# Performance work log

Measured on AMD Instinct MI355X. Metric: run time of the kernel, lower is better.

Reference implementation:

```python
import jax, jax.numpy as jnp
import numpy as np

ALPHA = 100.0
EPS = 1e-12  # matches torch F.normalize eps


def l2norm(v, axis):
    n = jnp.linalg.norm(v, axis=axis, keepdims=True)
    return v / jnp.maximum(n, EPS)


def setup_inputs() -> dict:
    key = jax.random.key(0)
    k1, k2 = jax.random.split(key)
    x = jax.random.normal(k1, (32, 512, 32, 32), dtype=jnp.float32)
    vocabs = jax.random.uniform(k2, (64, 512), dtype=jnp.float32)  # torch.rand init
    return {"x": x, "vocabs": vocabs}


def reference(x, vocabs):
    # x: [N, C, H, W]; vocabs: [K, C]
    N, C, H, W = x.shape
    K = vocabs.shape[0]
    x = l2norm(x, axis=1)                       # normalize descriptors over C
    xf = x.reshape(N, C, H * W)                 # [N, C, P]

    # 1x1 conv with weight = 2*alpha*vocabs, bias = -alpha*||vocabs||
    w = 2.0 * ALPHA * vocabs                    # [K, C]
    b = -ALPHA * jnp.linalg.norm(vocabs, axis=1)  # [K]
    logits = jnp.einsum('ncp,kc->nkp', xf, w) + b[None, :, None]
    a = jax.nn.softmax(logits, axis=1)          # soft assignment over K

    # Distributive rewrite of sum_p a[n,k,p]*(x[n,c,p] - vocabs[k,c])
    vlad = jnp.einsum('nkp,ncp->nkc', a, xf) - a.sum(-1)[:, :, None] * vocabs[None]
    vlad = l2norm(vlad, axis=2)                 # intra-normalization
    vlad = vlad.reshape(N, K * C)
    return l2norm(vlad, axis=1)
```

## Files before the change

kernel.cpp:

```cpp
#include <hip/hip_runtime.h>
#include <math.h>
#include <stdint.h>

#define ALPHA 100.0f
#define EPSN 1e-12f

typedef __attribute__((ext_vector_type(8))) short bf16x8;
typedef __attribute__((ext_vector_type(16))) float f32x16;
typedef __attribute__((ext_vector_type(4))) unsigned int u32x4;

static __device__ __forceinline__ uint32_t f2bf(float f) {
    uint32_t u = __builtin_bit_cast(uint32_t, f);
    return (u + 0x7FFFu + ((u >> 16) & 1u)) >> 16;
}
static __device__ __forceinline__ float bfhi(uint32_t u) {
    return __builtin_bit_cast(float, u & 0xFFFF0000u);
}
static __device__ __forceinline__ float bflo(uint32_t u) {
    return __builtin_bit_cast(float, u << 16);
}
static __device__ __forceinline__ uint32_t stage1(float f) {
    uint32_t hi = f2bf(f);
    uint32_t lo = f2bf(f - __builtin_bit_cast(float, hi << 16));
    return (hi << 16) | lo;
}
static __device__ __forceinline__ uint32_t packbf(float a, float b) {
    return f2bf(a) | (f2bf(b) << 16);
}
static __device__ __forceinline__ void lds_barrier() {
    asm volatile("s_waitcnt lgkmcnt(0)\n\ts_barrier" ::: "memory");
}

__global__ __launch_bounds__(64) void prep_kernel(const float* __restrict__ v,
                                                  unsigned short* __restrict__ vh,
                                                  unsigned short* __restrict__ vl,
                                                  float* __restrict__ bias,
                                                  float* __restrict__ az) {
    int k = blockIdx.x, lane = threadIdx.x;
    az[k * 64 + lane] = 0.f;
    const float* row = v + k * 512;
    float ssq = 0.f;
#pragma unroll
    for (int i = 0; i < 8; ++i) {
        int c = lane + 64 * i;
        float f = row[c];
        ssq = fmaf(f, f, ssq);
        uint32_t hi = f2bf(f);
        uint32_t lo = f2bf(f - __builtin_bit_cast(float, hi << 16));
        vh[k * 512 + c] = (unsigned short)hi;
        vl[k * 512 + c] = (unsigned short)lo;
    }
#pragma unroll
    for (int off = 32; off > 0; off >>= 1) ssq += __shfl_xor(ssq, off, 64);
    if (lane == 0) bias[k] = -ALPHA * sqrtf(ssq);
}

static __device__ __forceinline__ void a_load(float4& pxa, float4& pxb,
                                              u32x4& pvh, u32x4& pvl,
                                              const float* xg,
                                              const unsigned short* vhg,
                                              const unsigned short* vlg,
                                              int c0, int xr, int xq) {
    pxa = *(const float4*)(xg + (size_t)(c0 + xr) * 1024 + xq);
    pxb = *(const float4*)(xg + (size_t)(c0 + xr + 16) * 1024 + xq);
    pvh = *(const u32x4*)(vhg + c0);
    pvl = *(const u32x4*)(vlg + c0);
}
static __device__ __forceinline__ void a_stage(uint32_t* xsb, uint32_t* vhsb,
                                               uint32_t* vlsb, const float4 pxa,
                                               const float4 pxb, const u32x4 pvh,
                                               const u32x4 pvl, int xr, int xq,
                                               int vk, int vj) {
    *(uint2*)&xsb[xr * 66 + xq] = make_uint2(stage1(pxa.x), stage1(pxa.y));
    *(uint2*)&xsb[xr * 66 + xq + 2] = make_uint2(stage1(pxa.z), stage1(pxa.w));
    *(uint2*)&xsb[(xr + 16) * 66 + xq] = make_uint2(stage1(pxb.x), stage1(pxb.y));
    *(uint2*)&xsb[(xr + 16) * 66 + xq + 2] = make_uint2(stage1(pxb.z), stage1(pxb.w));
    int vb = vk * 18 + (vj >> 1);
    *(uint2*)&vhsb[vb] = make_uint2(pvh[0], pvh[1]);
    *(uint2*)&vhsb[vb + 2] = make_uint2(pvh[2], pvh[3]);
    *(uint2*)&vlsb[vb] = make_uint2(pvl[0], pvl[1]);
    *(uint2*)&vlsb[vb + 2] = make_uint2(pvl[2], pvl[3]);
}
static __device__ __forceinline__ void a_compute(const uint32_t* xsb,
                                                 const uint32_t* vhsb,
                                                 const uint32_t* vlsb,
                                                 f32x16& acc, float& ssq,
                                                 int kh, int ph, int h, int cl) {
#pragma unroll
    for (int s = 0; s < 2; ++s) {
        int va = (32 * kh + cl) * 18 + 8 * s + 4 * h;
        uint2 a0 = *(const uint2*)&vhsb[va];
        uint2 a1 = *(const uint2*)&vhsb[va + 2];
        uint2 b0 = *(const uint2*)&vlsb[va];
        uint2 b1 = *(const uint2*)&vlsb[va + 2];
        u32x4 ahp, alp;
        ahp[0] = a0.x; ahp[1] = a0.y; ahp[2] = a1.x; ahp[3] = a1.y;
        alp[0] = b0.x; alp[1] = b0.y; alp[2] = b1.x; alp[3] = b1.y;
        uint32_t wv[8];
#pragma unroll
        for (int j = 0; j < 8; ++j)
            wv[j] = xsb[(16 * s + 8 * h + j) * 66 + 32 * ph + cl];
#pragma unroll
        for (int j = 0; j < 8; ++j) {
            float xv = bfhi(wv[j]) + bflo(wv[j]);
            ssq = fmaf(xv, xv, ssq);
        }
        u32x4 bhp, blp;
#pragma unroll
        for (int q = 0; q < 4; ++q) {
            bhp[q] = (wv[2 * q] >> 16) | (wv[2 * q + 1] & 0xFFFF0000u);
            blp[q] = (wv[2 * q] & 0xFFFFu) | (wv[2 * q + 1] << 16);
        }
        bf16x8 ah = __builtin_bit_cast(bf16x8, ahp);
        bf16x8 al = __builtin_bit_cast(bf16x8, alp);
        bf16x8 bh = __builtin_bit_cast(bf16x8, bhp);
        bf16x8 bl = __builtin_bit_cast(bf16x8, blp);
        acc = __builtin_amdgcn_mfma_f32_32x32x16_bf16(ah, bh, acc, 0, 0, 0);
        acc = __builtin_amdgcn_mfma_f32_32x32x16_bf16(ah, bl, acc, 0, 0, 0);
        acc = __builtin_amdgcn_mfma_f32_32x32x16_bf16(al, bh, acc, 0, 0, 0);
    }
}

__global__ __launch_bounds__(256) void assign_kernel(
    const float* __restrict__ x, const unsigned short* __restrict__ vh,
    const unsigned short* __restrict__ vl, const float* __restrict__ bias,
    unsigned short* __restrict__ aT, float* __restrict__ asum) {
    __shared__ uint32_t xs[2][32 * 66];
    __shared__ uint32_t vhs[2][64 * 18];
    __shared__ uint32_t vls[2][64 * 18];
    __shared__ float bias_l[64];
    __shared__ float xch[2][2][32];

    int tid = threadIdx.x, bx = blockIdx.x;
    int n = bx >> 4, pblk = (bx & 15) << 6;
    int l = tid & 63, w = tid >> 6;
    int kh = w & 1, ph = w >> 1;
    int h = l >> 5, cl = l & 31;

    if (tid < 64) bias_l[tid] = bias[tid];

    int xr = tid >> 4, xq = (tid & 15) << 2;
    int vk = tid >> 2, vj = (tid & 3) << 3;

    const float* xg = x + (size_t)n * 524288 + pblk;
    const unsigned short* vhg = vh + vk * 512 + vj;
    const unsigned short* vlg = vl + vk * 512 + vj;

    f32x16 acc;
#pragma unroll
    for (int r = 0; r < 16; ++r) acc[r] = 0.f;
    float ssq = 0.f;

    float4 pxa[2], pxb[2];
    u32x4 pvh[2], pvl[2];
    a_load(pxa[0], pxb[0], pvh[0], pvl[0], xg, vhg, vlg, 0, xr, xq);
    a_load(pxa[1], pxb[1], pvh[1], pvl[1], xg, vhg, vlg, 32, xr, xq);
    __syncthreads();
    a_stage(xs[0], vhs[0], vls[0], pxa[0], pxb[0], pvh[0], pvl[0], xr, xq, vk, vj);
    lds_barrier();
#pragma unroll
    for (int cc = 0; cc < 8; ++cc) {
        a_stage(xs[1], vhs[1], vls[1], pxa[1], pxb[1], pvh[1], pvl[1], xr, xq, vk, vj);
        if (cc < 7)
            a_load(pxa[0], pxb[0], pvh[0], pvl[0], xg, vhg, vlg, (2 * cc + 2) << 5, xr, xq);
        a_compute(xs[0], vhs[0], vls[0], acc, ssq, kh, ph, h, cl);
        lds_barrier();
        if (cc < 7) {
            a_stage(xs[0], vhs[0], vls[0], pxa[0], pxb[0], pvh[0], pvl[0], xr, xq, vk, vj);
            a_load(pxa[1], pxb[1], pvh[1], pvl[1], xg, vhg, vlg, (2 * cc + 3) << 5, xr, xq);
        }
        a_compute(xs[1], vhs[1], vls[1], acc, ssq, kh, ph, h, cl);
        lds_barrier();
    }
    ssq += __shfl_xor(ssq, 32, 64);
    float sinv = 1.0f / fmaxf(sqrtf(ssq), EPSN);
    float twoAs = 2.0f * ALPHA * sinv;
    float e[16];
    float m = -INFINITY;
#pragma unroll
    for (int r = 0; r < 16; ++r) {
        int k = (r & 3) + 8 * (r >> 2) + 4 * h + 32 * kh;
        float lv = fmaf(twoAs, acc[r], bias_l[k]);
        e[r] = lv;
        m = fmaxf(m, lv);
    }
    m = fmaxf(m, __shfl_xor(m, 32, 64));
    __syncthreads();
    if (l < 32) xch[kh][ph][l] = m;
    __syncthreads();
    m = fmaxf(m, xch[1 - kh][ph][cl]);
    float ssum = 0.f;
#pragma unroll
    for (int r = 0; r < 16; ++r) {
        e[r] = expf(e[r] - m);
        ssum += e[r];
    }
    ssum += __shfl_xor(ssum, 32, 64);
    __syncthreads();
    if (l < 32) xch[kh][ph][l] = ssum;
    __syncthreads();
    ssum += xch[1 - kh][ph][cl];
    float rs = 1.0f / ssum;
    float a2s = rs * sinv;
    unsigned short* aTn = aT + (size_t)n * 65536 + pblk + 32 * ph + cl;
#pragma unroll
    for (int r = 0; r < 16; ++r) {
        int k = (r & 3) + 8 * (r >> 2) + 4 * h + 32 * kh;
        aTn[(size_t)k * 1024] = (unsigned short)f2bf(e[r] * a2s);
        float red = e[r] * rs;
#pragma unroll
        for (int off = 1; off <= 16; off <<= 1) red += __shfl_xor(red, off, 64);
        if (cl == 0) atomicAdd(&asum[n * 64 + k], red);
    }
}

static __device__ __forceinline__ void v_load(float4& qxa, float4& qxb,
                                              u32x4& qa0, u32x4& qa1,
                                              const float* xg,
                                              const unsigned short* ag, int p0) {
    qxa = *(const float4*)(xg + p0);
    qxb = *(const float4*)(xg + p0 + 32);
    qa0 = *(const u32x4*)(ag + p0);
    qa1 = *(const u32x4*)(ag + p0 + 8);
}
static __device__ __forceinline__ void v_stage(uint32_t* xtb, uint32_t* atb,
                                               const float4 qxa, const float4 qxb,
                                               const u32x4 qa0, const u32x4 qa1,
                                               int xr, int xq, int ak, int aj) {
    int xb = xr * 34 + (xq >> 1);
    *(uint2*)&xtb[xb] = make_uint2(packbf(qxa.x, qxa.y), packbf(qxa.z, qxa.w));
    *(uint2*)&xtb[xb + 16] = make_uint2(packbf(qxb.x, qxb.y), packbf(qxb.z, qxb.w));
    int ab = ak * 34 + (aj >> 1);
    *(uint2*)&atb[ab] = make_uint2(qa0[0], qa0[1]);
    *(uint2*)&atb[ab + 2] = make_uint2(qa0[2], qa0[3]);
    *(uint2*)&atb[ab + 4] = make_uint2(qa1[0], qa1[1]);
    *(uint2*)&atb[ab + 6] = make_uint2(qa1[2], qa1[3]);
}
static __device__ __forceinline__ void v_compute(const uint32_t* xtb,
                                                 const uint32_t* atb,
                                                 f32x16& acc, int kh, int h,
                                                 int cl) {
#pragma unroll
    for (int s = 0; s < 4; ++s) {
        int va = (32 * kh + cl) * 34 + 8 * s + 4 * h;
        uint2 f0 = *(const uint2*)&atb[va];
        uint2 f1 = *(const uint2*)&atb[va + 2];
        int vb = cl * 34 + 8 * s + 4 * h;
        uint2 g0 = *(const uint2*)&xtb[vb];
        uint2 g1 = *(const uint2*)&xtb[vb + 2];
        u32x4 afp, bfp;
        afp[0] = f0.x; afp[1] = f0.y; afp[2] = f1.x; afp[3] = f1.y;
        bfp[0] = g0.x; bfp[1] = g0.y; bfp[2] = g1.x; bfp[3] = g1.y;
        acc = __builtin_amdgcn_mfma_f32_32x32x16_bf16(
            __builtin_bit_cast(bf16x8, afp), __builtin_bit_cast(bf16x8, bfp),
            acc, 0, 0, 0);
    }
}

__global__ __launch_bounds__(256) void vlad_kernel(
    const float* __restrict__ x, const unsigned short* __restrict__ aT,
    const float* __restrict__ asum, const float* __restrict__ vocabs,
    float* __restrict__ out, float* __restrict__ knorm) {
    __shared__ uint32_t xt[2][32 * 34];
    __shared__ uint32_t at[2][64 * 34];
    __shared__ float cmb[2][64][16];
    __shared__ float asum_l[64];

    int tid = threadIdx.x, bx = blockIdx.x;
    int n = bx >> 4, cb = (bx & 15) << 5;
    int l = tid & 63, w = tid >> 6;
    int kh = w & 1, ps = w >> 1;
    int h = l >> 5, cl = l & 31;

    if (tid < 64) asum_l[tid] = asum[n * 64 + tid];

    int xr = tid >> 3, xq = (tid & 7) << 2;
    int ak = tid >> 2, aj = (tid & 3) << 4;

    const float* xg = x + (size_t)n * 524288 + (size_t)(cb + xr) * 1024 + xq;
    const unsigned short* ag = aT + (size_t)n * 65536 + (size_t)ak * 1024 + aj;

    f32x16 acc;
#pragma unroll
    for (int r = 0; r < 16; ++r) acc[r] = 0.f;

    float4 qxa[2], qxb[2];
    u32x4 qa0[2], qa1[2];
    v_load(qxa[0], qxb[0], qa0[0], qa1[0], xg, ag, 0);
    v_load(qxa[1], qxb[1], qa0[1], qa1[1], xg, ag, 64);
    __syncthreads();
    v_stage(xt[0], at[0], qxa[0], qxb[0], qa0[0], qa1[0], xr, xq, ak, aj);
    lds_barrier();
#pragma unroll
    for (int cc = 0; cc < 8; ++cc) {
        v_stage(xt[1], at[1], qxa[1], qxb[1], qa0[1], qa1[1], xr, xq, ak, aj);
        if (cc < 7)
            v_load(qxa[0], qxb[0], qa0[0], qa1[0], xg, ag, (2 * cc + 2) << 6);
        if (ps == 0) v_compute(xt[0], at[0], acc, kh, h, cl);
        lds_barrier();
        if (cc < 7) {
            v_stage(xt[0], at[0], qxa[0], qxb[0], qa0[0], qa1[0], xr, xq, ak, aj);
            v_load(qxa[1], qxb[1], qa0[1], qa1[1], xg, ag, (2 * cc + 3) << 6);
        }
        if (ps == 1) v_compute(xt[1], at[1], acc, kh, h, cl);
        lds_barrier();
    }
    __syncthreads();
    if (ps == 1) {
#pragma unroll
        for (int r = 0; r < 16; ++r) cmb[kh][l][r] = acc[r];
    }
    __syncthreads();
    if (ps == 0) {
#pragma unroll
        for (int r = 0; r < 16; ++r) {
            int k = (r & 3) + 8 * (r >> 2) + 4 * h + 32 * kh;
            int c = cb + cl;
            float val = acc[r] + cmb[kh][l][r];
            val = fmaf(-asum_l[k], vocabs[k * 512 + c], val);
            out[(size_t)n * 32768 + (size_t)k * 512 + c] = val;
            float t2 = val * val;
#pragma unroll
            for (int off = 1; off <= 16; off <<= 1) t2 += __shfl_xor(t2, off, 64);
            if (cl == 0) atomicAdd(&knorm[n * 64 + k], t2);
        }
    }
}

__global__ __launch_bounds__(256) void scale_kernel(float* __restrict__ out,
                                                    const float* __restrict__ knorm) {
    int n = blockIdx.y;
    int sb = blockIdx.x;
    int tid = threadIdx.x;
    __shared__ float sc[64];
    __shared__ float tots;
    if (tid < 64) {
        float kn = knorm[n * 64 + tid];
        float nk = sqrtf(kn);
        float inv = 1.0f / fmaxf(nk, EPSN);
        sc[tid] = inv;
        float t = nk * inv;
        float t2 = t * t;
#pragma unroll
        for (int off = 32; off > 0; off >>= 1) t2 += __shfl_xor(t2, off, 64);
        if (tid == 0) tots = t2;
    }
    __syncthreads();
    float invt = 1.0f / fmaxf(sqrtf(tots), EPSN);
    float* base = out + (size_t)n * 32768 + sb * 4096;
#pragma unroll
    for (int i = 0; i < 16; ++i) {
        int idx = tid + 256 * i;
        int k = (sb * 4096 + idx) >> 9;
        base[idx] *= sc[k] * invt;
    }
}

extern "C" void kernel_launch(void* const* d_in, const int* in_sizes, int n_in,
                              void* d_out, int out_size, void* d_ws, size_t ws_size,
                              hipStream_t stream) {
    const float* x = (const float*)d_in[0];
    const float* vocabs = (const float*)d_in[1];
    float* out = (float*)d_out;
    char* ws = (char*)d_ws;
    unsigned short* vh = (unsigned short*)(ws);
    unsigned short* vl = (unsigned short*)(ws + 65536);
    float* bias  = (float*)(ws + 131072);
    float* asum  = (float*)(ws + 131328);
    float* knorm = (float*)(ws + 139520);
    unsigned short* aT = (unsigned short*)(ws + 147712);

    prep_kernel<<<64, 64, 0, stream>>>(vocabs, vh, vl, bias, asum);
    assign_kernel<<<512, 256, 0, stream>>>(x, vh, vl, bias, aT, asum);
    vlad_kernel<<<512, 256, 0, stream>>>(x, aT, asum, vocabs, out, knorm);
    scale_kernel<<<dim3(8, 32), 256, 0, stream>>>(out, knorm);
}
```

Baseline: 136.7 us.

## Split x staging into pre-packed hi/lo LDS planes and compute norms at staging

The x tile is now staged in LDS as separate bf16 hi and lo planes, each word packing two adjacent channels. The MFMA B operands can then be read directly, with no per-word shuffle and unpack in the compute loop. The sum of squares for the L2 norm is accumulated in fp32 from the global loads during staging rather than rebuilt from bf16 pairs in compute. Reducing it now takes an extra LDS buffer and two block barriers before the softmax.

```diff
diff --git a/kernel.cpp b/kernel.cpp
--- a/kernel.cpp
+++ b/kernel.cpp
@@ -7,6 +7,7 @@
 
 typedef __attribute__((ext_vector_type(8))) short bf16x8;
 typedef __attribute__((ext_vector_type(16))) float f32x16;
+typedef __attribute__((ext_vector_type(4))) float f32x4;
 typedef __attribute__((ext_vector_type(4))) unsigned int u32x4;
 
 static __device__ __forceinline__ uint32_t f2bf(float f) {
@@ -18,11 +19,6 @@
 }
 static __device__ __forceinline__ float bflo(uint32_t u) {
     return __builtin_bit_cast(float, u << 16);
-}
-static __device__ __forceinline__ uint32_t stage1(float f) {
-    uint32_t hi = f2bf(f);
-    uint32_t lo = f2bf(f - __builtin_bit_cast(float, hi << 16));
-    return (hi << 16) | lo;
 }
 static __device__ __forceinline__ uint32_t packbf(float a, float b) {
     return f2bf(a) | (f2bf(b) << 16);
@@ -61,30 +57,43 @@
                                               const unsigned short* vhg,
                                               const unsigned short* vlg,
                                               int c0, int xr, int xq) {
-    pxa = *(const float4*)(xg + (size_t)(c0 + xr) * 1024 + xq);
-    pxb = *(const float4*)(xg + (size_t)(c0 + xr + 16) * 1024 + xq);
+    pxa = *(const float4*)(xg + (size_t)(c0 + 2 * xr) * 1024 + xq);
+    pxb = *(const float4*)(xg + (size_t)(c0 + 2 * xr + 1) * 1024 + xq);
     pvh = *(const u32x4*)(vhg + c0);
     pvl = *(const u32x4*)(vlg + c0);
 }
-static __device__ __forceinline__ void a_stage(uint32_t* xsb, uint32_t* vhsb,
-                                               uint32_t* vlsb, const float4 pxa,
-                                               const float4 pxb, const u32x4 pvh,
-                                               const u32x4 pvl, int xr, int xq,
-                                               int vk, int vj) {
-    *(uint2*)&xsb[xr * 66 + xq] = make_uint2(stage1(pxa.x), stage1(pxa.y));
-    *(uint2*)&xsb[xr * 66 + xq + 2] = make_uint2(stage1(pxa.z), stage1(pxa.w));
-    *(uint2*)&xsb[(xr + 16) * 66 + xq] = make_uint2(stage1(pxb.x), stage1(pxb.y));
-    *(uint2*)&xsb[(xr + 16) * 66 + xq + 2] = make_uint2(stage1(pxb.z), stage1(pxb.w));
+static __device__ __forceinline__ void a_stage(uint32_t* xhb, uint32_t* xlb,
+                                               uint32_t* vhsb, uint32_t* vlsb,
+                                               const float4 pxa, const float4 pxb,
+                                               const u32x4 pvh, const u32x4 pvl,
+                                               int xr, int xq, int vk, int vj,
+                                               f32x4& ssqv) {
+    float fa[4] = {pxa.x, pxa.y, pxa.z, pxa.w};
+    float fb[4] = {pxb.x, pxb.y, pxb.z, pxb.w};
+    u32x4 hp, lp;
+#pragma unroll
+    for (int i = 0; i < 4; ++i) {
+        uint32_t h0 = f2bf(fa[i]);
+        uint32_t l0 = f2bf(fa[i] - bfhi(h0 << 16));
+        uint32_t h1 = f2bf(fb[i]);
+        uint32_t l1 = f2bf(fb[i] - bfhi(h1 << 16));
+        hp[i] = h0 | (h1 << 16);
+        lp[i] = l0 | (l1 << 16);
+        ssqv[i] = fmaf(fa[i], fa[i], fmaf(fb[i], fb[i], ssqv[i]));
+    }
+    *(u32x4*)&xhb[xr * 68 + xq] = hp;
+    *(u32x4*)&xlb[xr * 68 + xq] = lp;
     int vb = vk * 18 + (vj >> 1);
     *(uint2*)&vhsb[vb] = make_uint2(pvh[0], pvh[1]);
     *(uint2*)&vhsb[vb + 2] = make_uint2(pvh[2], pvh[3]);
     *(uint2*)&vlsb[vb] = make_uint2(pvl[0], pvl[1]);
     *(uint2*)&vlsb[vb + 2] = make_uint2(pvl[2], pvl[3]);
 }
-static __device__ __forceinline__ void a_compute(const uint32_t* xsb,
+static __device__ __forceinline__ void a_compute(const uint32_t* xhb,
+                                                 const uint32_t* xlb,
                                                  const uint32_t* vhsb,
                                                  const uint32_t* vlsb,
-                                                 f32x16& acc, float& ssq,
+                                                 f32x16& acc,
                                                  int kh, int ph, int h, int cl) {
 #pragma unroll
     for (int s = 0; s < 2; ++s) {
@@ -96,20 +105,12 @@
         u32x4 ahp, alp;
         ahp[0] = a0.x; ahp[1] = a0.y; ahp[2] = a1.x; ahp[3] = a1.y;
         alp[0] = b0.x; alp[1] = b0.y; alp[2] = b1.x; alp[3] = b1.y;
-        uint32_t wv[8];
-#pragma unroll
-        for (int j = 0; j < 8; ++j)
-            wv[j] = xsb[(16 * s + 8 * h + j) * 66 + 32 * ph + cl];
-#pragma unroll
-        for (int j = 0; j < 8; ++j) {
-            float xv = bfhi(wv[j]) + bflo(wv[j]);
-            ssq = fmaf(xv, xv, ssq);
-        }
+        int xb = (8 * s + 4 * h) * 68 + 32 * ph + cl;
         u32x4 bhp, blp;
 #pragma unroll
         for (int q = 0; q < 4; ++q) {
-            bhp[q] = (wv[2 * q] >> 16) | (wv[2 * q + 1] & 0xFFFF0000u);
-            blp[q] = (wv[2 * q] & 0xFFFFu) | (wv[2 * q + 1] << 16);
+            bhp[q] = xhb[xb + q * 68];
+            blp[q] = xlb[xb + q * 68];
         }
         bf16x8 ah = __builtin_bit_cast(bf16x8, ahp);
         bf16x8 al = __builtin_bit_cast(bf16x8, alp);
@@ -125,11 +126,14 @@
     const float* __restrict__ x, const unsigned short* __restrict__ vh,
     const unsigned short* __restrict__ vl, const float* __restrict__ bias,
     unsigned short* __restrict__ aT, float* __restrict__ asum) {
-    __shared__ uint32_t xs[2][32 * 66];
+    __shared__ uint32_t xhs[2][16 * 68];
+    __shared__ uint32_t xls[2][16 * 68];
     __shared__ uint32_t vhs[2][64 * 18];
     __shared__ uint32_t vls[2][64 * 18];
     __shared__ float bias_l[64];
     __shared__ float xch[2][2][32];
+    __shared__ float ssq_s[16 * 68];
+    __shared__ float ssq_l[64];
 
     int tid = threadIdx.x, bx = blockIdx.x;
     int n = bx >> 4, pblk = (bx & 15) << 6;
@@ -149,30 +153,44 @@
     f32x16 acc;
 #pragma unroll
     for (int r = 0; r < 16; ++r) acc[r] = 0.f;
-    float ssq = 0.f;
+    f32x4 ssqv;
+#pragma unroll
+    for (int i = 0; i < 4; ++i) ssqv[i] = 0.f;
 
     float4 pxa[2], pxb[2];
     u32x4 pvh[2], pvl[2];
     a_load(pxa[0], pxb[0], pvh[0], pvl[0], xg, vhg, vlg, 0, xr, xq);
     a_load(pxa[1], pxb[1], pvh[1], pvl[1], xg, vhg, vlg, 32, xr, xq);
     __syncthreads();
-    a_stage(xs[0], vhs[0], vls[0], pxa[0], pxb[0], pvh[0], pvl[0], xr, xq, vk, vj);
+    a_stage(xhs[0], xls[0], vhs[0], vls[0], pxa[0], pxb[0], pvh[0], pvl[0],
+            xr, xq, vk, vj, ssqv);
     lds_barrier();
 #pragma unroll
     for (int cc = 0; cc < 8; ++cc) {
-        a_stage(xs[1], vhs[1], vls[1], pxa[1], pxb[1], pvh[1], pvl[1], xr, xq, vk, vj);
+        a_stage(xhs[1], xls[1], vhs[1], vls[1], pxa[1], pxb[1], pvh[1], pvl[1],
+                xr, xq, vk, vj, ssqv);
         if (cc < 7)
             a_load(pxa[0], pxb[0], pvh[0], pvl[0], xg, vhg, vlg, (2 * cc + 2) << 5, xr, xq);
-        a_compute(xs[0], vhs[0], vls[0], acc, ssq, kh, ph, h, cl);
+        a_compute(xhs[0], xls[0], vhs[0], vls[0], acc, kh, ph, h, cl);
         lds_barrier();
         if (cc < 7) {
-            a_stage(xs[0], vhs[0], vls[0], pxa[0], pxb[0], pvh[0], pvl[0], xr, xq, vk, vj);
+            a_stage(xhs[0], xls[0], vhs[0], vls[0], pxa[0], pxb[0], pvh[0], pvl[0],
+                    xr, xq, vk, vj, ssqv);
             a_load(pxa[1], pxb[1], pvh[1], pvl[1], xg, vhg, vlg, (2 * cc + 3) << 5, xr, xq);
         }
-        a_compute(xs[1], vhs[1], vls[1], acc, ssq, kh, ph, h, cl);
+        a_compute(xhs[1], xls[1], vhs[1], vls[1], acc, kh, ph, h, cl);
         lds_barrier();
     }
-    ssq += __shfl_xor(ssq, 32, 64);
+    *(f32x4*)&ssq_s[xr * 68 + xq] = ssqv;
+    __syncthreads();
+    if (tid < 64) {
+        float s = 0.f;
+#pragma unroll
+        for (int r2 = 0; r2 < 16; ++r2) s += ssq_s[r2 * 68 + tid];
+        ssq_l[tid] = s;
+    }
+    __syncthreads();
+    float ssq = ssq_l[32 * ph + cl];
     float sinv = 1.0f / fmaxf(sqrtf(ssq), EPSN);
     float twoAs = 2.0f * ALPHA * sinv;
     float e[16];
```

Result: no change. 139.3 us (+1.9%).

## Use wave-private LDS staging and register-resident vocab fragments in assign kernel

Applied to the files above, without the earlier changes.

Each wave now stages only its own 32-pixel slice of x into private double-buffered LDS, split into separate hi and lo planes. This removes block-wide barriers from the channel loop. Vocab hi/lo fragments are loaded straight from global memory into registers instead of through LDS, and the per-pixel sum of squares is gathered during staging with a shuffle reduction at the end. In exchange, the two waves that share a pixel slice each load and convert the same x data, doubling that global traffic and conversion work.

```diff
diff --git a/kernel.cpp b/kernel.cpp
--- a/kernel.cpp
+++ b/kernel.cpp
@@ -7,6 +7,7 @@
 
 typedef __attribute__((ext_vector_type(8))) short bf16x8;
 typedef __attribute__((ext_vector_type(16))) float f32x16;
+typedef __attribute__((ext_vector_type(4))) float f32x4;
 typedef __attribute__((ext_vector_type(4))) unsigned int u32x4;
 
 static __device__ __forceinline__ uint32_t f2bf(float f) {
@@ -15,14 +16,6 @@
 }
 static __device__ __forceinline__ float bfhi(uint32_t u) {
     return __builtin_bit_cast(float, u & 0xFFFF0000u);
-}
-static __device__ __forceinline__ float bflo(uint32_t u) {
-    return __builtin_bit_cast(float, u << 16);
-}
-static __device__ __forceinline__ uint32_t stage1(float f) {
-    uint32_t hi = f2bf(f);
-    uint32_t lo = f2bf(f - __builtin_bit_cast(float, hi << 16));
-    return (hi << 16) | lo;
 }
 static __device__ __forceinline__ uint32_t packbf(float a, float b) {
     return f2bf(a) | (f2bf(b) << 16);
@@ -55,79 +48,13 @@
     if (lane == 0) bias[k] = -ALPHA * sqrtf(ssq);
 }
 
-static __device__ __forceinline__ void a_load(float4& pxa, float4& pxb,
-                                              u32x4& pvh, u32x4& pvl,
-                                              const float* xg,
-                                              const unsigned short* vhg,
-                                              const unsigned short* vlg,
-                                              int c0, int xr, int xq) {
-    pxa = *(const float4*)(xg + (size_t)(c0 + xr) * 1024 + xq);
-    pxb = *(const float4*)(xg + (size_t)(c0 + xr + 16) * 1024 + xq);
-    pvh = *(const u32x4*)(vhg + c0);
-    pvl = *(const u32x4*)(vlg + c0);
-}
-static __device__ __forceinline__ void a_stage(uint32_t* xsb, uint32_t* vhsb,
-                                               uint32_t* vlsb, const float4 pxa,
-                                               const float4 pxb, const u32x4 pvh,
-                                               const u32x4 pvl, int xr, int xq,
-                                               int vk, int vj) {
-    *(uint2*)&xsb[xr * 66 + xq] = make_uint2(stage1(pxa.x), stage1(pxa.y));
-    *(uint2*)&xsb[xr * 66 + xq + 2] = make_uint2(stage1(pxa.z), stage1(pxa.w));
-    *(uint2*)&xsb[(xr + 16) * 66 + xq] = make_uint2(stage1(pxb.x), stage1(pxb.y));
-    *(uint2*)&xsb[(xr + 16) * 66 + xq + 2] = make_uint2(stage1(pxb.z), stage1(pxb.w));
-    int vb = vk * 18 + (vj >> 1);
-    *(uint2*)&vhsb[vb] = make_uint2(pvh[0], pvh[1]);
-    *(uint2*)&vhsb[vb + 2] = make_uint2(pvh[2], pvh[3]);
-    *(uint2*)&vlsb[vb] = make_uint2(pvl[0], pvl[1]);
-    *(uint2*)&vlsb[vb + 2] = make_uint2(pvl[2], pvl[3]);
-}
-static __device__ __forceinline__ void a_compute(const uint32_t* xsb,
-                                                 const uint32_t* vhsb,
-                                                 const uint32_t* vlsb,
-                                                 f32x16& acc, float& ssq,
-                                                 int kh, int ph, int h, int cl) {
-#pragma unroll
-    for (int s = 0; s < 2; ++s) {
-        int va = (32 * kh + cl) * 18 + 8 * s + 4 * h;
-        uint2 a0 = *(const uint2*)&vhsb[va];
-        uint2 a1 = *(const uint2*)&vhsb[va + 2];
-        uint2 b0 = *(const uint2*)&vlsb[va];
-        uint2 b1 = *(const uint2*)&vlsb[va + 2];
-        u32x4 ahp, alp;
-        ahp[0] = a0.x; ahp[1] = a0.y; ahp[2] = a1.x; ahp[3] = a1.y;
-        alp[0] = b0.x; alp[1] = b0.y; alp[2] = b1.x; alp[3] = b1.y;
-        uint32_t wv[8];
-#pragma unroll
-        for (int j = 0; j < 8; ++j)
-            wv[j] = xsb[(16 * s + 8 * h + j) * 66 + 32 * ph + cl];
-#pragma unroll
-        for (int j = 0; j < 8; ++j) {
-            float xv = bfhi(wv[j]) + bflo(wv[j]);
-            ssq = fmaf(xv, xv, ssq);
-        }
-        u32x4 bhp, blp;
-#pragma unroll
-        for (int q = 0; q < 4; ++q) {
-            bhp[q] = (wv[2 * q] >> 16) | (wv[2 * q + 1] & 0xFFFF0000u);
-            blp[q] = (wv[2 * q] & 0xFFFFu) | (wv[2 * q + 1] << 16);
-        }
-        bf16x8 ah = __builtin_bit_cast(bf16x8, ahp);
-        bf16x8 al = __builtin_bit_cast(bf16x8, alp);
-        bf16x8 bh = __builtin_bit_cast(bf16x8, bhp);
-        bf16x8 bl = __builtin_bit_cast(bf16x8, blp);
-        acc = __builtin_amdgcn_mfma_f32_32x32x16_bf16(ah, bh, acc, 0, 0, 0);
-        acc = __builtin_amdgcn_mfma_f32_32x32x16_bf16(ah, bl, acc, 0, 0, 0);
-        acc = __builtin_amdgcn_mfma_f32_32x32x16_bf16(al, bh, acc, 0, 0, 0);
-    }
-}
-
 __global__ __launch_bounds__(256) void assign_kernel(
     const float* __restrict__ x, const unsigned short* __restrict__ vh,
     const unsigned short* __restrict__ vl, const float* __restrict__ bias,
     unsigned short* __restrict__ aT, float* __restrict__ asum) {
-    __shared__ uint32_t xs[2][32 * 66];
-    __shared__ uint32_t vhs[2][64 * 18];
-    __shared__ uint32_t vls[2][64 * 18];
+    __shared__ uint32_t xph[4][2][16 * 36];
+    __shared__ uint32_t xpl[4][2][16 * 36];
+    __shared__ float ssqw[4][32];
     __shared__ float bias_l[64];
     __shared__ float xch[2][2][32];
 
@@ -136,43 +63,123 @@
     int l = tid & 63, w = tid >> 6;
     int kh = w & 1, ph = w >> 1;
     int h = l >> 5, cl = l & 31;
+    int c8 = l & 7, j = (l >> 3) & 7;
 
     if (tid < 64) bias_l[tid] = bias[tid];
 
-    int xr = tid >> 4, xq = (tid & 15) << 2;
-    int vk = tid >> 2, vj = (tid & 3) << 3;
-
-    const float* xg = x + (size_t)n * 524288 + pblk;
-    const unsigned short* vhg = vh + vk * 512 + vj;
-    const unsigned short* vlg = vl + vk * 512 + vj;
+    const float* xg = x + (size_t)n * 524288 + pblk + 32 * ph + 4 * c8;
+    const unsigned short* vhg = vh + (size_t)(32 * kh + cl) * 512 + 8 * h;
+    const unsigned short* vlg = vl + (size_t)(32 * kh + cl) * 512 + 8 * h;
+
+    uint32_t* bh0 = xph[w][0];
+    uint32_t* bh1 = xph[w][1];
+    uint32_t* bl0 = xpl[w][0];
+    uint32_t* bl1 = xpl[w][1];
 
     f32x16 acc;
 #pragma unroll
     for (int r = 0; r < 16; ++r) acc[r] = 0.f;
-    float ssq = 0.f;
-
-    float4 pxa[2], pxb[2];
-    u32x4 pvh[2], pvl[2];
-    a_load(pxa[0], pxb[0], pvh[0], pvl[0], xg, vhg, vlg, 0, xr, xq);
-    a_load(pxa[1], pxb[1], pvh[1], pvl[1], xg, vhg, vlg, 32, xr, xq);
-    __syncthreads();
-    a_stage(xs[0], vhs[0], vls[0], pxa[0], pxb[0], pvh[0], pvl[0], xr, xq, vk, vj);
-    lds_barrier();
-#pragma unroll
-    for (int cc = 0; cc < 8; ++cc) {
-        a_stage(xs[1], vhs[1], vls[1], pxa[1], pxb[1], pvh[1], pvl[1], xr, xq, vk, vj);
-        if (cc < 7)
-            a_load(pxa[0], pxb[0], pvh[0], pvl[0], xg, vhg, vlg, (2 * cc + 2) << 5, xr, xq);
-        a_compute(xs[0], vhs[0], vls[0], acc, ssq, kh, ph, h, cl);
-        lds_barrier();
-        if (cc < 7) {
-            a_stage(xs[0], vhs[0], vls[0], pxa[0], pxb[0], pvh[0], pvl[0], xr, xq, vk, vj);
-            a_load(pxa[1], pxb[1], pvh[1], pvl[1], xg, vhg, vlg, (2 * cc + 3) << 5, xr, xq);
+    f32x4 ssqv;
+#pragma unroll
+    for (int i = 0; i < 4; ++i) ssqv[i] = 0.f;
+
+    float4 xv[2][4];
+    u32x4 vfh[2][2], vfl[2][2];
+
+#define A_LOADX(slot, c0)                                                      \
+    {                                                                          \
+        xv[slot][0] = *(const float4*)(xg + (size_t)((c0) + 2 * j) * 1024);    \
+        xv[slot][1] = *(const float4*)(xg + (size_t)((c0) + 2 * j + 1) * 1024);\
+        xv[slot][2] = *(const float4*)(xg + (size_t)((c0) + 2 * j + 16) * 1024);\
+        xv[slot][3] = *(const float4*)(xg + (size_t)((c0) + 2 * j + 17) * 1024);\
+    }
+#define A_LOADV(slot, c0)                                                      \
+    {                                                                          \
+        vfh[slot][0] = *(const u32x4*)(vhg + (c0));                            \
+        vfh[slot][1] = *(const u32x4*)(vhg + (c0) + 16);                       \
+        vfl[slot][0] = *(const u32x4*)(vlg + (c0));                            \
+        vfl[slot][1] = *(const u32x4*)(vlg + (c0) + 16);                       \
+    }
+#define A_STAGE(bh_, bl_, slot)                                                \
+    {                                                                          \
+        _Pragma("unroll") for (int ps0 = 0; ps0 < 2; ++ps0) {                  \
+            float fa[4] = {xv[slot][2 * ps0].x, xv[slot][2 * ps0].y,           \
+                           xv[slot][2 * ps0].z, xv[slot][2 * ps0].w};          \
+            float fb[4] = {xv[slot][2 * ps0 + 1].x, xv[slot][2 * ps0 + 1].y,   \
+                           xv[slot][2 * ps0 + 1].z, xv[slot][2 * ps0 + 1].w};  \
+            u32x4 hp, lp;                                                      \
+            _Pragma("unroll") for (int i = 0; i < 4; ++i) {                    \
+                uint32_t h0 = f2bf(fa[i]);                                     \
+                uint32_t l0 = f2bf(fa[i] - bfhi(h0 << 16));                    \
+                uint32_t h1 = f2bf(fb[i]);                                     \
+                uint32_t l1 = f2bf(fb[i] - bfhi(h1 << 16));                    \
+                hp[i] = h0 | (h1 << 16);                                       \
+                lp[i] = l0 | (l1 << 16);                                       \
+                ssqv[i] = fmaf(fa[i], fa[i], fmaf(fb[i], fb[i], ssqv[i]));     \
+            }                                                                  \
+            *(u32x4*)&(bh_)[(j + 8 * ps0) * 36 + 4 * c8] = hp;                 \
+            *(u32x4*)&(bl_)[(j + 8 * ps0) * 36 + 4 * c8] = lp;                 \
+        }                                                                      \
+    }
+#define A_COMPUTE(bh_, bl_, slot)                                              \
+    {                                                                          \
+        _Pragma("unroll") for (int s = 0; s < 2; ++s) {                        \
+            int xb = (8 * s + 4 * h) * 36 + cl;                                \
+            u32x4 bhp, blp;                                                    \
+            _Pragma("unroll") for (int q = 0; q < 4; ++q) {                    \
+                bhp[q] = (bh_)[xb + q * 36];                                   \
+                blp[q] = (bl_)[xb + q * 36];                                   \
+            }                                                                  \
+            bf16x8 ah = __builtin_bit_cast(bf16x8, vfh[slot][s]);              \
+            bf16x8 al = __builtin_bit_cast(bf16x8, vfl[slot][s]);              \
+            bf16x8 xbh = __builtin_bit_cast(bf16x8, bhp);                      \
+            bf16x8 xbl = __builtin_bit_cast(bf16x8, blp);                      \
+            acc = __builtin_amdgcn_mfma_f32_32x32x16_bf16(ah, xbh, acc, 0, 0, 0);\
+            acc = __builtin_amdgcn_mfma_f32_32x32x16_bf16(ah, xbl, acc, 0, 0, 0);\
+            acc = __builtin_amdgcn_mfma_f32_32x32x16_bf16(al, xbh, acc, 0, 0, 0);\
+        }                                                                      \
+    }
+
+    A_LOADX(0, 0);
+    A_LOADV(0, 0);
+    A_LOADX(1, 32);
+    A_LOADV(1, 32);
+    __syncthreads();
+    A_STAGE(bh0, bl0, 0);
+#pragma unroll
+    for (int i = 0; i < 16; ++i) {
+        if ((i & 1) == 0) {
+            A_COMPUTE(bh0, bl0, 0);
+            if (i < 15) A_STAGE(bh1, bl1, 1);
+            if (i < 14) {
+                A_LOADX(0, (i + 2) * 32);
+                A_LOADV(0, (i + 2) * 32);
+            }
+        } else {
+            A_COMPUTE(bh1, bl1, 1);
+            if (i < 15) A_STAGE(bh0, bl0, 0);
+            if (i < 14) {
+                A_LOADX(1, (i + 2) * 32);
+                A_LOADV(1, (i + 2) * 32);
+            }
         }
-        a_compute(xs[1], vhs[1], vls[1], acc, ssq, kh, ph, h, cl);
-        lds_barrier();
-    }
-    ssq += __shfl_xor(ssq, 32, 64);
+    }
+#undef A_LOADX
+#undef A_LOADV
+#undef A_STAGE
+#undef A_COMPUTE
+
+#pragma unroll
+    for (int i = 0; i < 4; ++i) {
+        float v = ssqv[i];
+        v += __shfl_xor(v, 8, 64);
+        v += __shfl_xor(v, 16, 64);
+        v += __shfl_xor(v, 32, 64);
+        ssqv[i] = v;
+    }
+    if (l < 8) *(f32x4*)&ssqw[w][4 * c8] = ssqv;
+    float ssq = ssqw[w][cl];
+
     float sinv = 1.0f / fmaxf(sqrtf(ssq), EPSN);
     float twoAs = 2.0f * ALPHA * sinv;
     float e[16];
```

New measurement: 149.5 us. +9.3%, slower.
